# Performance work log

Measured on AMD Instinct MI355X. Metric: run time of the kernel, lower is better.

Reference implementation:

```python
import jax, jax.numpy as jnp
import numpy as np

BATCH, T, ALPHABET, N_STATES = 64, 4096, 32, 128


def setup_inputs() -> dict:
    key = jax.random.key(0)
    k1, k2, k3, k4 = jax.random.split(key, 4)
    # one-hot emission sequences (DNA-style categorical observations)
    tokens = jax.random.randint(k1, (BATCH, T), 0, ALPHABET)
    inputs = jax.nn.one_hot(tokens, ALPHABET, dtype=jnp.float32)  # [B, T, A]
    A_logits = jax.random.normal(k2, (N_STATES, N_STATES), dtype=jnp.float32)
    B_logits = jax.random.normal(k3, (ALPHABET, N_STATES), dtype=jnp.float32)
    I_logits = jax.random.normal(k4, (N_STATES,), dtype=jnp.float32)
    return {"inputs": inputs, "A_logits": A_logits, "B_logits": B_logits, "I_logits": I_logits}


def reference(inputs, A_logits, B_logits, I_logits):
    # Softmax-parameterized HMM: rows of A sum to 1 (transitions), columns of B
    # sum to 1 over the alphabet (emissions per state), I is the initial dist.
    A = jax.nn.softmax(A_logits, axis=1)          # [S, S]
    Bm = jax.nn.softmax(B_logits, axis=0)          # [A, S]
    I = jax.nn.softmax(I_logits)                   # [S]

    # Per-step emission likelihoods for every state (batched lookup via one-hot matmul)
    E = jnp.einsum('bta,as->bts', inputs, Bm)      # [B, T, S]

    # t = 0: alpha_0 = I * E_0, normalized; loglik accumulates the scale factors
    alpha = I[None, :] * E[:, 0]                   # [B, S]
    s = jnp.sum(alpha, axis=1, keepdims=True)      # [B, 1]
    alpha = alpha / s
    loglik = jnp.log(s[:, 0])                      # [B]

    def step(carry, Et):
        alpha, loglik = carry
        alpha = jnp.matmul(alpha, A) * Et          # [B, S]
        s = jnp.sum(alpha, axis=1, keepdims=True)
        alpha = alpha / s
        loglik = loglik + jnp.log(s[:, 0])
        return (alpha, loglik), None

    E_rest = jnp.swapaxes(E[:, 1:], 0, 1)          # time-major [T-1, B, S]
    (alpha, loglik), _ = jax.lax.scan(step, (alpha, loglik), E_rest)
    return loglik                                   # loglik_state, shape [B]
```

## Files before the change

kernel.cpp:

```cpp
#include <hip/hip_runtime.h>
#include <math.h>

#define BATCH 64
#define T 4096
#define ALPH 32
#define NS 128
#define MB 16
#define NGRP 4
#define NCHUNK 256
#define CL 16
#define WARM 16

typedef __bf16 bf16x8 __attribute__((ext_vector_type(8)));
typedef short  short8 __attribute__((ext_vector_type(8)));
typedef float  f32x4  __attribute__((ext_vector_type(4)));

#define WS_FRAG 0
#define WS_BME  8192
#define WS_I    10240
#define WS_PART 10368
#define WS_TOK_F 26752

static __device__ inline unsigned short f2u(float f) {
    __bf16 b = (__bf16)f;
    return __builtin_bit_cast(unsigned short, b);
}


__global__ __launch_bounds__(256) void setup_kernel(const float* __restrict__ onehot,
                                                    const float* __restrict__ A_logits,
                                                    const float* __restrict__ B_logits,
                                                    const float* __restrict__ I_logits,
                                                    float* __restrict__ ws,
                                                    unsigned char* __restrict__ tok) {
    unsigned short* frag = (unsigned short*)(ws + WS_FRAG);
    unsigned short* Bme  = (unsigned short*)(ws + WS_BME);
    float* I_ws = ws + WS_I;
    const int blk = blockIdx.x;
    const int tid = threadIdx.x;

    if (blk < 1024) {
        int b = blk >> 4;
        int t = (blk & 15) * 256 + tid;
        const float4* p = (const float4*)(onehot + ((size_t)b * T + t) * ALPH);
        int tk = 0;
        #pragma unroll
        for (int q = 0; q < 8; ++q) {
            float4 v = p[q];
            if (v.x > 0.5f) tk = 4 * q + 0;
            if (v.y > 0.5f) tk = 4 * q + 1;
            if (v.z > 0.5f) tk = 4 * q + 2;
            if (v.w > 0.5f) tk = 4 * q + 3;
        }
        tok[(size_t)b * T + t] = (unsigned char)tk;
        return;
    }

    if (blk == 1024 + NS) {
        if (tid < NS) {
            int s = tid;
            float m = -1e30f;
            for (int a = 0; a < ALPH; ++a) m = fmaxf(m, B_logits[a * NS + s]);
            float sum = 0.f;
            for (int a = 0; a < ALPH; ++a) sum += expf(B_logits[a * NS + s] - m);
            float inv = 1.0f / sum;
            int idx = (s & 15) * 8 + (s >> 4);
            for (int a = 0; a < ALPH; ++a)
                Bme[a * NS + idx] = f2u(expf(B_logits[a * NS + s] - m) * inv);
        }
        __shared__ float redm[4];
        __shared__ float reds[4];
        float x = (tid < NS) ? I_logits[tid] : -1e30f;
        float m = x;
        #pragma unroll
        for (int off = 1; off < 64; off <<= 1) m = fmaxf(m, __shfl_xor(m, off));
        int wid = tid >> 6;
        if ((tid & 63) == 0) redm[wid] = m;
        __syncthreads();
        m = fmaxf(fmaxf(redm[0], redm[1]), fmaxf(redm[2], redm[3]));
        float e = (tid < NS) ? expf(x - m) : 0.0f;
        float sg = e;
        #pragma unroll
        for (int off = 1; off < 64; off <<= 1) sg += __shfl_xor(sg, off);
        if ((tid & 63) == 0) reds[wid] = sg;
        __syncthreads();
        float total = (reds[0] + reds[1]) + (reds[2] + reds[3]);
        if (tid < NS) {
            int n = tid;
            int p = (n >> 5) * 32 + (n & 15) * 2 + ((n >> 4) & 1);
            I_ws[p] = e / total;
        }
        return;
    }

    int rho = blk - 1024;
    __shared__ float redm[4];
    __shared__ float reds[4];
    float x = (tid < NS) ? A_logits[rho * NS + tid] : -1e30f;
    float m = x;
    #pragma unroll
    for (int off = 1; off < 64; off <<= 1) m = fmaxf(m, __shfl_xor(m, off));
    int wid = tid >> 6;
    if ((tid & 63) == 0) redm[wid] = m;
    __syncthreads();
    m = fmaxf(fmaxf(redm[0], redm[1]), fmaxf(redm[2], redm[3]));
    float e = (tid < NS) ? expf(x - m) : 0.0f;
    float sg = e;
    #pragma unroll
    for (int off = 1; off < 64; off <<= 1) sg += __shfl_xor(sg, off);
    if ((tid & 63) == 0) reds[wid] = sg;
    __syncthreads();
    float total = (reds[0] + reds[1]) + (reds[2] + reds[3]);
    if (tid < NS) {
        float v = e / total;
        int gamma = tid;
        int kc   = rho >> 5;
        int jlow = (rho >> 4) & 1;
        int quad = (rho >> 2) & 3;
        int j    = (rho & 3) * 2 + jlow;
        int nt   = gamma >> 4;
        int col  = gamma & 15;
        int lane = quad * 16 + col;
        int fid  = kc * 8 + nt;
        frag[fid * 512 + lane * 8 + j] = f2u(v);
    }
}

__global__ __launch_bounds__(256, 1) void hmm_kernel(const float* __restrict__ ws,
                                                     const unsigned char* __restrict__ tok_g,
                                                     float* __restrict__ part) {
    const unsigned short* Bme_g = (const unsigned short*)(ws + WS_BME);
    const float* I_ws = ws + WS_I;
    const char* frag_g = (const char*)(ws + WS_FRAG);

    const int c    = blockIdx.x;
    const int tid  = threadIdx.x;
    const int g    = tid >> 6;
    const int lane = tid & 63;
    const int quad = lane >> 4;
    const int col  = lane & 15;

    __shared__ unsigned short Bme_lds[ALPH * NS];
    __shared__ __align__(16) short alpha_lds[NGRP][2][MB * 136];
    __shared__ unsigned char tok_lds[(CL + WARM) * BATCH];

    const int t0     = (c == 0) ? 0 : (c * CL - WARM);
    const int nsteps = (c == 0) ? (CL - 1) : (CL + WARM - 1);
    const int ntok   = nsteps + 1;
    const int resetj = (c == 0) ? -1 : WARM;

    {
        const unsigned* src = (const unsigned*)Bme_g;
        unsigned* dst = (unsigned*)Bme_lds;
        #pragma unroll
        for (int i = 0; i < 8; ++i) dst[i * 256 + tid] = src[i * 256 + tid];
    }
    {
        int b = tid & 63, half = tid >> 6;
        if (half * 8 < ntok) {
            uint2 v = *(const uint2*)(tok_g + (size_t)b * T + t0 + half * 8);
            unsigned lo = v.x, hi = v.y;
            #pragma unroll
            for (int i = 0; i < 4; ++i) {
                tok_lds[(half * 8 + i) * 64 + b]     = (unsigned char)((lo >> (8 * i)) & 255);
                tok_lds[(half * 8 + 4 + i) * 64 + b] = (unsigned char)((hi >> (8 * i)) & 255);
            }
        }
    }
    bf16x8 bfr[32];
    #pragma unroll
    for (int fid = 0; fid < 32; ++fid)
        bfr[fid] = __builtin_bit_cast(bf16x8, *(const short8*)(frag_g + fid * 1024 + lane * 16));

    __syncthreads();

    {
        #pragma unroll
        for (int it = 0; it < 32; ++it) {
            int idx = it * 64 + lane;
            int m = idx >> 7, p = idx & 127;
            float val;
            if (c == 0) {
                int tk0 = tok_lds[0 * 64 + g * 16 + m];
                int nt = ((p >> 5) << 1) + (p & 1);
                int cc = (p >> 1) & 15;
                float bm = (float)__builtin_bit_cast(__bf16, Bme_lds[tk0 * NS + cc * 8 + nt]);
                val = I_ws[p] * bm;
            } else {
                val = 1.0f;
            }
            alpha_lds[g][0][m * 136 + p] = (short)f2u(val);
        }
    }

    float loglik = 0.0f;

    for (int j = 1; j <= nsteps; ++j) {
        const int rb = (j + 1) & 1;
        const int wb = j & 1;
        const bool do_norm = ((j & 7) == 0);

        unsigned tokp = *(const unsigned*)&tok_lds[j * 64 + g * 16 + quad * 4];
        bf16x8 efr[4];
        #pragma unroll
        for (int r = 0; r < 4; ++r) {
            int tk = (tokp >> (8 * r)) & 255;
            efr[r] = *(const bf16x8*)&Bme_lds[tk * NS + col * 8];
        }

        const short* ap = &alpha_lds[g][rb][col * 136 + quad * 8];
        bf16x8 afr[4];
        #pragma unroll
        for (int kc = 0; kc < 4; ++kc)
            afr[kc] = *(const bf16x8*)(ap + kc * 32);

        f32x4 acc[8];
        #pragma unroll
        for (int nt = 0; nt < 8; ++nt) acc[nt] = (f32x4){0.f, 0.f, 0.f, 0.f};
        #pragma unroll
        for (int nt = 0; nt < 8; ++nt) {
            #pragma unroll
            for (int kc = 0; kc < 4; ++kc)
                acc[nt] = __builtin_amdgcn_mfma_f32_16x16x32_bf16(afr[kc], bfr[kc * 8 + nt], acc[nt], 0, 0, 0);
        }

        float inv[4] = {1.0f, 1.0f, 1.0f, 1.0f};
        if (do_norm) {
            float asum = 0.f;
            #pragma unroll
            for (int kc = 0; kc < 4; ++kc) {
                #pragma unroll
                for (int jj = 0; jj < 8; ++jj) asum += (float)afr[kc][jj];
            }
            asum += __shfl_xor(asum, 16);
            asum += __shfl_xor(asum, 32);
            float lg = __logf(asum);
            loglik = (j == resetj) ? 0.0f : (loglik + lg);
            #pragma unroll
            for (int r = 0; r < 4; ++r)
                inv[r] = __builtin_amdgcn_rcpf(__shfl(asum, quad * 4 + r));
        }

        #pragma unroll
        for (int r = 0; r < 4; ++r) {
            unsigned* wrow = (unsigned*)&alpha_lds[g][wb][(quad * 4 + r) * 136];
            #pragma unroll
            for (int a = 0; a < 4; ++a) {
                float x0 = acc[2 * a][r]     * (float)efr[r][2 * a]     * inv[r];
                float x1 = acc[2 * a + 1][r] * (float)efr[r][2 * a + 1] * inv[r];
                wrow[a * 16 + col] = (unsigned)f2u(x0) | ((unsigned)f2u(x1) << 16);
            }
        }
    }

    {
        const short* ap = &alpha_lds[g][nsteps & 1][col * 136 + quad * 8];
        float tot = 0.f;
        #pragma unroll
        for (int kc = 0; kc < 4; ++kc) {
            bf16x8 av = *(const bf16x8*)(ap + kc * 32);
            #pragma unroll
            for (int jj = 0; jj < 8; ++jj) tot += (float)av[jj];
        }
        tot += __shfl_xor(tot, 16);
        tot += __shfl_xor(tot, 32);
        if (quad == 0)
            part[c * 64 + g * 16 + col] = loglik + __logf(tot);
    }
}

__global__ __launch_bounds__(256) void reduce_kernel(const float* __restrict__ part,
                                                     float* __restrict__ out) {
    __shared__ float red[4][64];
    int b = threadIdx.x & 63;
    int cg = threadIdx.x >> 6;
    float s = 0.f;
    #pragma unroll 4
    for (int k = 0; k < 64; ++k)
        s += part[(cg * 64 + k) * 64 + b];
    red[cg][b] = s;
    __syncthreads();
    if (threadIdx.x < 64)
        out[threadIdx.x] = (red[0][threadIdx.x] + red[1][threadIdx.x]) +
                           (red[2][threadIdx.x] + red[3][threadIdx.x]);
}

extern "C" void kernel_launch(void* const* d_in, const int* in_sizes, int n_in,
                              void* d_out, int out_size, void* d_ws, size_t ws_size,
                              hipStream_t stream) {
    const float* onehot   = (const float*)d_in[0];
    const float* A_logits = (const float*)d_in[1];
    const float* B_logits = (const float*)d_in[2];
    const float* I_logits = (const float*)d_in[3];
    float* ws  = (float*)d_ws;
    float* out = (float*)d_out;
    unsigned char* tok = (unsigned char*)(ws + WS_TOK_F);

    setup_kernel<<<dim3(1024 + NS + 1), dim3(256), 0, stream>>>(
        onehot, A_logits, B_logits, I_logits, ws, tok);
    hmm_kernel<<<dim3(NCHUNK), dim3(256), 0, stream>>>(ws, tok, ws + WS_PART);
    reduce_kernel<<<dim3(1), dim3(256), 0, stream>>>(ws + WS_PART, out);
}
```

Before: 114.1 us.

## Halve chunk length to 512 chunks, single-buffer alpha, atomic-add partial logliks

Splits the time axis into 512 chunks of 8 steps instead of 256 chunks of 16, so there are twice as many blocks, each with a shorter serial dependency chain. Launch bounds now allow 2 blocks per CU. Alpha is kept in one LDS buffer instead of a double buffer, and bf16 rounding is done with a bit-add-and-permute. The separate reduce kernel is replaced by atomicAdd into the output, which setup_kernel zeroes first. The trade-off is that warmup steps make up a larger share of each chunk's work, and the float atomics make the order of the final sum nondeterministic.

```diff
diff --git a/kernel.cpp b/kernel.cpp
--- a/kernel.cpp
+++ b/kernel.cpp
@@ -7,8 +7,8 @@
 #define NS 128
 #define MB 16
 #define NGRP 4
-#define NCHUNK 256
-#define CL 16
+#define NCHUNK 512
+#define CL 8
 #define WARM 16
 
 typedef __bf16 bf16x8 __attribute__((ext_vector_type(8)));
@@ -18,8 +18,7 @@
 #define WS_FRAG 0
 #define WS_BME  8192
 #define WS_I    10240
-#define WS_PART 10368
-#define WS_TOK_F 26752
+#define WS_TOK_F 10368
 
 static __device__ inline unsigned short f2u(float f) {
     __bf16 b = (__bf16)f;
@@ -32,6 +31,7 @@
                                                     const float* __restrict__ B_logits,
                                                     const float* __restrict__ I_logits,
                                                     float* __restrict__ ws,
+                                                    float* __restrict__ out,
                                                     unsigned char* __restrict__ tok) {
     unsigned short* frag = (unsigned short*)(ws + WS_FRAG);
     unsigned short* Bme  = (unsigned short*)(ws + WS_BME);
@@ -67,6 +67,8 @@
             int idx = (s & 15) * 8 + (s >> 4);
             for (int a = 0; a < ALPH; ++a)
                 Bme[a * NS + idx] = f2u(expf(B_logits[a * NS + s] - m) * inv);
+        } else if (tid < NS + BATCH) {
+            out[tid - NS] = 0.0f;
         }
         __shared__ float redm[4];
         __shared__ float reds[4];
@@ -126,9 +128,9 @@
     }
 }
 
-__global__ __launch_bounds__(256, 1) void hmm_kernel(const float* __restrict__ ws,
+__global__ __launch_bounds__(256, 2) void hmm_kernel(const float* __restrict__ ws,
                                                      const unsigned char* __restrict__ tok_g,
-                                                     float* __restrict__ part) {
+                                                     float* __restrict__ out) {
     const unsigned short* Bme_g = (const unsigned short*)(ws + WS_BME);
     const float* I_ws = ws + WS_I;
     const char* frag_g = (const char*)(ws + WS_FRAG);
@@ -141,13 +143,15 @@
     const int col  = lane & 15;
 
     __shared__ unsigned short Bme_lds[ALPH * NS];
-    __shared__ __align__(16) short alpha_lds[NGRP][2][MB * 136];
+    __shared__ __align__(16) short alpha_lds[NGRP][MB * 136];
     __shared__ unsigned char tok_lds[(CL + WARM) * BATCH];
 
-    const int t0     = (c == 0) ? 0 : (c * CL - WARM);
-    const int nsteps = (c == 0) ? (CL - 1) : (CL + WARM - 1);
+    const int t0u    = c * CL - WARM;
+    const int t0     = (t0u < 0) ? 0 : t0u;
+    const bool exact = (t0 == 0);
+    const int nsteps = (c + 1) * CL - 1 - t0;
     const int ntok   = nsteps + 1;
-    const int resetj = (c == 0) ? -1 : WARM;
+    const int resetj = c * CL - t0;
 
     {
         const unsigned* src = (const unsigned*)Bme_g;
@@ -180,7 +184,7 @@
             int idx = it * 64 + lane;
             int m = idx >> 7, p = idx & 127;
             float val;
-            if (c == 0) {
+            if (exact) {
                 int tk0 = tok_lds[0 * 64 + g * 16 + m];
                 int nt = ((p >> 5) << 1) + (p & 1);
                 int cc = (p >> 1) & 15;
@@ -189,16 +193,14 @@
             } else {
                 val = 1.0f;
             }
-            alpha_lds[g][0][m * 136 + p] = (short)f2u(val);
+            alpha_lds[g][m * 136 + p] = (short)f2u(val);
         }
     }
 
     float loglik = 0.0f;
 
     for (int j = 1; j <= nsteps; ++j) {
-        const int rb = (j + 1) & 1;
-        const int wb = j & 1;
-        const bool do_norm = ((j & 7) == 0);
+        const bool do_norm = ((j & 7) == 0) || (j == resetj);
 
         unsigned tokp = *(const unsigned*)&tok_lds[j * 64 + g * 16 + quad * 4];
         bf16x8 efr[4];
@@ -208,7 +210,7 @@
             efr[r] = *(const bf16x8*)&Bme_lds[tk * NS + col * 8];
         }
 
-        const short* ap = &alpha_lds[g][rb][col * 136 + quad * 8];
+        const short* ap = &alpha_lds[g][col * 136 + quad * 8];
         bf16x8 afr[4];
         #pragma unroll
         for (int kc = 0; kc < 4; ++kc)
@@ -224,7 +226,14 @@
                 acc[nt] = __builtin_amdgcn_mfma_f32_16x16x32_bf16(afr[kc], bfr[kc * 8 + nt], acc[nt], 0, 0, 0);
         }
 
-        float inv[4] = {1.0f, 1.0f, 1.0f, 1.0f};
+        float vv[4][8];
+        #pragma unroll
+        for (int r = 0; r < 4; ++r) {
+            #pragma unroll
+            for (int i = 0; i < 8; ++i)
+                vv[r][i] = acc[i][r] * (float)efr[r][i];
+        }
+
         if (do_norm) {
             float asum = 0.f;
             #pragma unroll
@@ -237,24 +246,27 @@
             float lg = __logf(asum);
             loglik = (j == resetj) ? 0.0f : (loglik + lg);
             #pragma unroll
-            for (int r = 0; r < 4; ++r)
-                inv[r] = __builtin_amdgcn_rcpf(__shfl(asum, quad * 4 + r));
+            for (int r = 0; r < 4; ++r) {
+                float iv = __builtin_amdgcn_rcpf(__shfl(asum, quad * 4 + r));
+                #pragma unroll
+                for (int i = 0; i < 8; ++i) vv[r][i] *= iv;
+            }
         }
 
         #pragma unroll
         for (int r = 0; r < 4; ++r) {
-            unsigned* wrow = (unsigned*)&alpha_lds[g][wb][(quad * 4 + r) * 136];
+            unsigned* wrow = (unsigned*)&alpha_lds[g][(quad * 4 + r) * 136];
             #pragma unroll
             for (int a = 0; a < 4; ++a) {
-                float x0 = acc[2 * a][r]     * (float)efr[r][2 * a]     * inv[r];
-                float x1 = acc[2 * a + 1][r] * (float)efr[r][2 * a + 1] * inv[r];
-                wrow[a * 16 + col] = (unsigned)f2u(x0) | ((unsigned)f2u(x1) << 16);
-            }
-        }
-    }
-
-    {
-        const short* ap = &alpha_lds[g][nsteps & 1][col * 136 + quad * 8];
+                unsigned u0 = __builtin_bit_cast(unsigned, vv[r][2 * a])     + 0x8000u;
+                unsigned u1 = __builtin_bit_cast(unsigned, vv[r][2 * a + 1]) + 0x8000u;
+                wrow[a * 16 + col] = __builtin_amdgcn_perm(u1, u0, 0x07060302u);
+            }
+        }
+    }
+
+    {
+        const short* ap = &alpha_lds[g][col * 136 + quad * 8];
         float tot = 0.f;
         #pragma unroll
         for (int kc = 0; kc < 4; ++kc) {
@@ -265,24 +277,8 @@
         tot += __shfl_xor(tot, 16);
         tot += __shfl_xor(tot, 32);
         if (quad == 0)
-            part[c * 64 + g * 16 + col] = loglik + __logf(tot);
-    }
-}
-
-__global__ __launch_bounds__(256) void reduce_kernel(const float* __restrict__ part,
-                                                     float* __restrict__ out) {
-    __shared__ float red[4][64];
-    int b = threadIdx.x & 63;
-    int cg = threadIdx.x >> 6;
-    float s = 0.f;
-    #pragma unroll 4
-    for (int k = 0; k < 64; ++k)
-        s += part[(cg * 64 + k) * 64 + b];
-    red[cg][b] = s;
-    __syncthreads();
-    if (threadIdx.x < 64)
-        out[threadIdx.x] = (red[0][threadIdx.x] + red[1][threadIdx.x]) +
-                           (red[2][threadIdx.x] + red[3][threadIdx.x]);
+            atomicAdd(out + g * 16 + col, loglik + __logf(tot));
+    }
 }
 
 extern "C" void kernel_launch(void* const* d_in, const int* in_sizes, int n_in,
@@ -297,7 +293,6 @@
     unsigned char* tok = (unsigned char*)(ws + WS_TOK_F);
 
     setup_kernel<<<dim3(1024 + NS + 1), dim3(256), 0, stream>>>(
-        onehot, A_logits, B_logits, I_logits, ws, tok);
-    hmm_kernel<<<dim3(NCHUNK), dim3(256), 0, stream>>>(ws, tok, ws + WS_PART);
-    reduce_kernel<<<dim3(1), dim3(256), 0, stream>>>(ws + WS_PART, out);
-}
+        onehot, A_logits, B_logits, I_logits, ws, out, tok);
+    hmm_kernel<<<dim3(NCHUNK), dim3(256), 0, stream>>>(ws, tok, out);
+}
```

Measured after the change: 112.9 us. No clear change (-1.1%).
